# Optimization experiments

Measured on AMD Instinct MI355X. Metric: run time of the kernel, lower is better.

## Reference

```python
import jax, jax.numpy as jnp
import numpy as np

B, NQ, NKV, D = 2, 2048, 2048, 1024
N_HEADS = 16
D_H = D // N_HEADS


def setup_inputs() -> dict:
    key = jax.random.key(0)
    ks = jax.random.split(key, 10)
    s = 0.02  # weight init scale
    return {
        "q": jax.random.normal(ks[0], (B, NQ, D), jnp.float32),
        "kv": jax.random.normal(ks[1], (B, NKV, D), jnp.float32),
        "Wq": jax.random.normal(ks[2], (D, D), jnp.float32) * s,
        "bq": jnp.zeros((D,), jnp.float32),
        "Wk": jax.random.normal(ks[3], (D, D), jnp.float32) * s,
        "bk": jnp.zeros((D,), jnp.float32),
        "Wv": jax.random.normal(ks[4], (D, D), jnp.float32) * s,
        "bv": jnp.zeros((D,), jnp.float32),
        "Wo": jax.random.normal(ks[5], (D, D), jnp.float32) * s,
        "bo": jnp.zeros((D,), jnp.float32),
    }


def reference(q, kv, Wq, bq, Wk, bk, Wv, bv, Wo, bo):
    # Linear projections (torch Linear: x @ W.T + b)
    qh = q @ Wq.T + bq   # [B, NQ, D]
    kh = kv @ Wk.T + bk  # [B, NKV, D]
    vh = kv @ Wv.T + bv  # [B, NKV, D]
    # Split heads: [B, N, H, d_h]
    qh = qh.reshape(B, NQ, N_HEADS, D_H)
    kh = kh.reshape(B, NKV, N_HEADS, D_H)
    vh = vh.reshape(B, NKV, N_HEADS, D_H)
    scale = 1.0 / jnp.sqrt(jnp.asarray(D_H, qh.dtype))
    # QK^T per head: [B, H, NQ, NKV]
    scores = jnp.einsum("bqhd,bkhd->bhqk", qh, kh) * scale
    att = jax.nn.softmax(scores, axis=-1)
    # dropout p=0.0 -> identity
    out = jnp.einsum("bhqk,bkhd->bqhd", att, vh)  # [B, NQ, H, d_h]
    out = out.reshape(B, NQ, D)
    return out @ Wo.T + bo
```

## Files before the change

### kernel.cpp

```cpp
#include <hip/hip_runtime.h>
#include <cstddef>
#include <cstdint>

using half4v  = __attribute__((ext_vector_type(4))) _Float16;
using half8   = __attribute__((ext_vector_type(8))) _Float16;
using floatx4 = __attribute__((ext_vector_type(4))) float;

#define B_   2
#define NQ_  2048
#define DM   1024
#define NH_  16
#define DH_  64
#define NTILES 32

__device__ __forceinline__ void async16(const _Float16* g, _Float16* l) {
    __builtin_amdgcn_global_load_lds(
        (const __attribute__((address_space(1))) unsigned int*)g,
        (__attribute__((address_space(3))) unsigned int*)l, 16, 0, 0);
}

__global__ __launch_bounds__(256) void cvt_all(
        const float* __restrict__ q,  const float* __restrict__ kv,
        const float* __restrict__ wq, const float* __restrict__ wk,
        const float* __restrict__ wv, const float* __restrict__ wo,
        _Float16* __restrict__ dq,  _Float16* __restrict__ dkv,
        _Float16* __restrict__ dwq, _Float16* __restrict__ dwk,
        _Float16* __restrict__ dwv, _Float16* __restrict__ dwo) {
    int blk = blockIdx.x;
    const float* s;
    _Float16* d;
    int base;
    if (blk < 2048)      { s = q;  d = dq;  base = blk; }
    else if (blk < 4096) { s = kv; d = dkv; base = blk - 2048; }
    else if (blk < 4608) { s = wq; d = dwq; base = blk - 4096; }
    else if (blk < 5120) { s = wk; d = dwk; base = blk - 4608; }
    else if (blk < 5632) { s = wv; d = dwv; base = blk - 5120; }
    else                 { s = wo; d = dwo; base = blk - 5632; }
    int i = base * 256 + threadIdx.x;
    const float4* s4 = (const float4*)s;
    float4 a = s4[2 * i], b = s4[2 * i + 1];
    half8 h;
    h[0] = (_Float16)a.x; h[1] = (_Float16)a.y; h[2] = (_Float16)a.z; h[3] = (_Float16)a.w;
    h[4] = (_Float16)b.x; h[5] = (_Float16)b.y; h[6] = (_Float16)b.z; h[7] = (_Float16)b.w;
    ((half8*)d)[i] = h;
}

__global__ __launch_bounds__(256, 3) void proj_qkv(
        const _Float16* __restrict__ q16, const _Float16* __restrict__ kv16,
        const _Float16* __restrict__ wqp, const _Float16* __restrict__ wkp,
        const _Float16* __restrict__ wvp,
        const float* __restrict__ bqp, const float* __restrict__ bkp,
        const float* __restrict__ bvp,
        _Float16* __restrict__ qh, _Float16* __restrict__ kh,
        _Float16* __restrict__ vt) {
    __shared__ _Float16 As[128 * 64];
    __shared__ _Float16 Bs[128 * 64];

    const int which = blockIdx.x >> 8;
    const int sub = blockIdx.x & 255;
    const _Float16* A = (which == 0) ? q16 : kv16;
    const _Float16* W = (which == 0) ? wqp : (which == 1) ? wkp : wvp;
    const float* bias = (which == 0) ? bqp : (which == 1) ? bkp : bvp;

    const int t = threadIdx.x;
    const int w = t >> 6, lane = t & 63;
    const int r16 = lane & 15, quad = lane >> 4;
    const int bn = sub & 7, bm = sub >> 3;
    const int m0 = bm * 128, n0 = bn * 128;
    const int wm = w >> 1, wn = w & 1;

    floatx4 acc[4][4];
#pragma unroll
    for (int i = 0; i < 4; i++)
#pragma unroll
        for (int j = 0; j < 4; j++)
#pragma unroll
            for (int r = 0; r < 4; r++) acc[i][j][r] = 0.f;

    const int ph0 = quad ^ (r16 & 7), ph1 = ph0 ^ 4;

    for (int k0 = 0; k0 < DM; k0 += 64) {
        __syncthreads();
#pragma unroll
        for (int i = 0; i < 4; i++) {
            int P = i * 256 + t;
            int m = P >> 3, c = (P & 7) ^ (m & 7);
            async16(A + (size_t)(m0 + m) * DM + k0 + c * 8, &As[P * 8]);
            async16(W + (size_t)(n0 + m) * DM + k0 + c * 8, &Bs[P * 8]);
        }
        asm volatile("s_waitcnt vmcnt(0)" ::: "memory");
        __syncthreads();

        half8 af[4][2], bf[4][2];
#pragma unroll
        for (int mi = 0; mi < 4; mi++) {
            int m = wm * 64 + mi * 16 + r16;
            af[mi][0] = ((const half8*)As)[m * 8 + ph0];
            af[mi][1] = ((const half8*)As)[m * 8 + ph1];
        }
#pragma unroll
        for (int ni = 0; ni < 4; ni++) {
            int n = wn * 64 + ni * 16 + r16;
            bf[ni][0] = ((const half8*)Bs)[n * 8 + ph0];
            bf[ni][1] = ((const half8*)Bs)[n * 8 + ph1];
        }
#pragma unroll
        for (int kd = 0; kd < 2; kd++)
#pragma unroll
            for (int mi = 0; mi < 4; mi++)
#pragma unroll
                for (int ni = 0; ni < 4; ni++)
                    acc[mi][ni] = __builtin_amdgcn_mfma_f32_16x16x32_f16(
                        af[mi][kd], bf[ni][kd], acc[mi][ni], 0, 0, 0);
    }

    if (which < 2) {
        _Float16* C = (which == 0) ? qh : kh;
        const float esc = (which == 0) ? 0.125f : 1.0f;
#pragma unroll
        for (int mi = 0; mi < 4; mi++)
#pragma unroll
            for (int r = 0; r < 4; r++) {
                int row = m0 + wm * 64 + mi * 16 + quad * 4 + r;
#pragma unroll
                for (int ni = 0; ni < 4; ni++) {
                    int col = n0 + wn * 64 + ni * 16 + r16;
                    C[(size_t)row * DM + col] = (_Float16)((acc[mi][ni][r] + bias[col]) * esc);
                }
            }
    } else {
#pragma unroll
        for (int mi = 0; mi < 4; mi++) {
            int krow = m0 + wm * 64 + mi * 16 + quad * 4;
            int bb = krow >> 11, kk = krow & 2047;
#pragma unroll
            for (int ni = 0; ni < 4; ni++) {
                int col = n0 + wn * 64 + ni * 16 + r16;
                int hh = col >> 6, dd = col & 63;
                float bv = bias[col];
                half4v pk;
#pragma unroll
                for (int r = 0; r < 4; r++) pk[r] = (_Float16)(acc[mi][ni][r] + bv);
                *(half4v*)&vt[((size_t)((bb * NH_ + hh) * DH_ + dd)) * NQ_ + kk] = pk;
            }
        }
    }
}

__global__ __launch_bounds__(256, 2) void attn_mfma(const _Float16* __restrict__ Qg,
                                                    const _Float16* __restrict__ Kg,
                                                    const _Float16* __restrict__ Vt,
                                                    _Float16* __restrict__ Og) {
    __shared__ _Float16 Ps[128 * 64];
    __shared__ _Float16 Ks[2][64 * 64];
    __shared__ _Float16 Vs[2][64 * 64];

    const int t = threadIdx.x, w = t >> 6, lane = t & 63;
    const int r16 = lane & 15, quad = lane >> 4;
    const int qt = blockIdx.x & 15;
    const int bh = blockIdx.x >> 4;
    const int b = bh >> 4, h = bh & 15;

    const _Float16* qbase = Qg + (size_t)(b * NQ_ + qt * 128) * DM + h * DH_;
    const _Float16* kbase = Kg + (size_t)(b * NQ_) * DM + h * DH_;
    const _Float16* vbase = Vt + (size_t)bh * DH_ * NQ_;

#pragma unroll
    for (int i = 0; i < 4; i++) {
        int P = i * 256 + t;
        int m = P >> 3, c = (P & 7) ^ (m & 7);
        async16(qbase + (size_t)m * DM + c * 8, &Ps[P * 8]);
    }
#pragma unroll
    for (int i = 0; i < 2; i++) {
        int P = i * 256 + t;
        int m = P >> 3, c = (P & 7) ^ (m & 7);
        async16(kbase + (size_t)m * DM + c * 8, &Ks[0][P * 8]);
        async16(vbase + (size_t)m * NQ_ + c * 8, &Vs[0][P * 8]);
    }
    asm volatile("s_waitcnt vmcnt(0)" ::: "memory");
    __syncthreads();

    const int ph0 = quad ^ (r16 & 7), ph1 = ph0 ^ 4;
    half8 Qf[2][2];
#pragma unroll
    for (int mi = 0; mi < 2; mi++) {
        int m = w * 32 + mi * 16 + r16;
        Qf[mi][0] = ((const half8*)Ps)[m * 8 + ph0];
        Qf[mi][1] = ((const half8*)Ps)[m * 8 + ph1];
    }

    floatx4 oaccT[2][4];
    float lacc[2] = {0.f, 0.f};
#pragma unroll
    for (int mi = 0; mi < 2; mi++)
#pragma unroll
        for (int nd = 0; nd < 4; nd++)
#pragma unroll
            for (int r = 0; r < 4; r++) oaccT[mi][nd][r] = 0.f;

    for (int kt = 0; kt < NTILES; kt++) {
        const int cur = kt & 1;
        asm volatile("s_waitcnt vmcnt(0)" ::: "memory");
        __syncthreads();

        if (kt + 1 < NTILES) {
            const int nxt = cur ^ 1;
#pragma unroll
            for (int i = 0; i < 2; i++) {
                int P = i * 256 + t;
                int m = P >> 3, c = (P & 7) ^ (m & 7);
                async16(kbase + (size_t)((kt + 1) * 64 + m) * DM + c * 8, &Ks[nxt][P * 8]);
                async16(vbase + (size_t)m * NQ_ + (kt + 1) * 64 + c * 8, &Vs[nxt][P * 8]);
            }
        }

        floatx4 sacc[2][4];
#pragma unroll
        for (int mi = 0; mi < 2; mi++)
#pragma unroll
            for (int nk = 0; nk < 4; nk++)
#pragma unroll
                for (int r = 0; r < 4; r++) sacc[mi][nk][r] = 0.f;
#pragma unroll
        for (int kd = 0; kd < 2; kd++)
#pragma unroll
            for (int nk = 0; nk < 4; nk++) {
                half8 kf = ((const half8*)Ks[cur])[(nk * 16 + r16) * 8 + (kd ? ph1 : ph0)];
                sacc[0][nk] = __builtin_amdgcn_mfma_f32_16x16x32_f16(kf, Qf[0][kd], sacc[0][nk], 0, 0, 0);
                sacc[1][nk] = __builtin_amdgcn_mfma_f32_16x16x32_f16(kf, Qf[1][kd], sacc[1][nk], 0, 0, 0);
            }

#pragma unroll
        for (int mi = 0; mi < 2; mi++) {
            int q = w * 32 + mi * 16 + r16;
#pragma unroll
            for (int nk = 0; nk < 4; nk++) {
                float p0 = __expf(sacc[mi][nk][0]);
                float p1 = __expf(sacc[mi][nk][1]);
                float p2 = __expf(sacc[mi][nk][2]);
                float p3 = __expf(sacc[mi][nk][3]);
                lacc[mi] += (p0 + p1) + (p2 + p3);
                half4v pk;
                pk[0] = (_Float16)p0; pk[1] = (_Float16)p1;
                pk[2] = (_Float16)p2; pk[3] = (_Float16)p3;
                int phys = (nk * 2 + (quad >> 1)) ^ (r16 & 7);
                *(half4v*)&Ps[q * 64 + phys * 8 + (quad & 1) * 4] = pk;
            }
        }

#pragma unroll
        for (int ks = 0; ks < 2; ks++) {
            half8 pf[2];
#pragma unroll
            for (int mi = 0; mi < 2; mi++) {
                int q = w * 32 + mi * 16 + r16;
                pf[mi] = ((const half8*)Ps)[q * 8 + ((ks * 4 + quad) ^ (r16 & 7))];
            }
#pragma unroll
            for (int nd = 0; nd < 4; nd++) {
                half8 vf = ((const half8*)Vs[cur])[(nd * 16 + r16) * 8 + ((ks * 4 + quad) ^ (r16 & 7))];
                oaccT[0][nd] = __builtin_amdgcn_mfma_f32_16x16x32_f16(vf, pf[0], oaccT[0][nd], 0, 0, 0);
                oaccT[1][nd] = __builtin_amdgcn_mfma_f32_16x16x32_f16(vf, pf[1], oaccT[1][nd], 0, 0, 0);
            }
        }
    }

#pragma unroll
    for (int mi = 0; mi < 2; mi++) {
        float l = lacc[mi];
        l += __shfl_xor(l, 16);
        l += __shfl_xor(l, 32);
        float inv = 1.f / l;
        int qrow = b * NQ_ + qt * 128 + w * 32 + mi * 16 + r16;
#pragma unroll
        for (int nd = 0; nd < 4; nd++) {
            half4v o;
#pragma unroll
            for (int r = 0; r < 4; r++) o[r] = (_Float16)(oaccT[mi][nd][r] * inv);
            *(half4v*)&Og[(size_t)qrow * DM + h * DH_ + nd * 16 + quad * 4] = o;
        }
    }
}

__global__ __launch_bounds__(256, 2) void gemm_o(const _Float16* __restrict__ A,
                                                 const _Float16* __restrict__ W,
                                                 const float* __restrict__ bias,
                                                 float* __restrict__ C) {
    __shared__ _Float16 As[128 * 64];
    __shared__ _Float16 Bs[64 * 64];

    const int t = threadIdx.x;
    const int w = t >> 6, lane = t & 63;
    const int r16 = lane & 15, quad = lane >> 4;
    const int bn = blockIdx.x & 15, bm = blockIdx.x >> 4;
    const int m0 = bm * 128, n0 = bn * 64;
    const int wm = w >> 1, wn = w & 1;

    floatx4 acc[4][2];
#pragma unroll
    for (int i = 0; i < 4; i++)
#pragma unroll
        for (int j = 0; j < 2; j++)
#pragma unroll
            for (int r = 0; r < 4; r++) acc[i][j][r] = 0.f;

    const int ph0 = quad ^ (r16 & 7), ph1 = ph0 ^ 4;

    for (int k0 = 0; k0 < DM; k0 += 64) {
        __syncthreads();
#pragma unroll
        for (int i = 0; i < 4; i++) {
            int P = i * 256 + t;
            int m = P >> 3, c = (P & 7) ^ (m & 7);
            async16(A + (size_t)(m0 + m) * DM + k0 + c * 8, &As[P * 8]);
        }
#pragma unroll
        for (int i = 0; i < 2; i++) {
            int P = i * 256 + t;
            int m = P >> 3, c = (P & 7) ^ (m & 7);
            async16(W + (size_t)(n0 + m) * DM + k0 + c * 8, &Bs[P * 8]);
        }
        asm volatile("s_waitcnt vmcnt(0)" ::: "memory");
        __syncthreads();

        half8 af[4][2], bf[2][2];
#pragma unroll
        for (int mi = 0; mi < 4; mi++) {
            int m = wm * 64 + mi * 16 + r16;
            af[mi][0] = ((const half8*)As)[m * 8 + ph0];
            af[mi][1] = ((const half8*)As)[m * 8 + ph1];
        }
#pragma unroll
        for (int ni = 0; ni < 2; ni++) {
            int n = wn * 32 + ni * 16 + r16;
            bf[ni][0] = ((const half8*)Bs)[n * 8 + ph0];
            bf[ni][1] = ((const half8*)Bs)[n * 8 + ph1];
        }
#pragma unroll
        for (int kd = 0; kd < 2; kd++)
#pragma unroll
            for (int mi = 0; mi < 4; mi++)
#pragma unroll
                for (int ni = 0; ni < 2; ni++)
                    acc[mi][ni] = __builtin_amdgcn_mfma_f32_16x16x32_f16(
                        af[mi][kd], bf[ni][kd], acc[mi][ni], 0, 0, 0);
    }

#pragma unroll
    for (int mi = 0; mi < 4; mi++)
#pragma unroll
        for (int r = 0; r < 4; r++) {
            int row = m0 + wm * 64 + mi * 16 + quad * 4 + r;
#pragma unroll
            for (int ni = 0; ni < 2; ni++) {
                int col = n0 + wn * 32 + ni * 16 + r16;
                C[(size_t)row * DM + col] = acc[mi][ni][r] + bias[col];
            }
        }
}

extern "C" void kernel_launch(void* const* d_in, const int* in_sizes, int n_in,
                              void* d_out, int out_size, void* d_ws, size_t ws_size,
                              hipStream_t stream) {
    const float* q  = (const float*)d_in[0];
    const float* kv = (const float*)d_in[1];
    const float* Wq = (const float*)d_in[2];
    const float* bq = (const float*)d_in[3];
    const float* Wk = (const float*)d_in[4];
    const float* bk = (const float*)d_in[5];
    const float* Wv = (const float*)d_in[6];
    const float* bv = (const float*)d_in[7];
    const float* Wo = (const float*)d_in[8];
    const float* bo = (const float*)d_in[9];

    char* ws = (char*)d_ws;
    _Float16* q16  = (_Float16*)(ws);
    _Float16* kv16 = (_Float16*)(ws + (size_t)(8  << 20));
    _Float16* w16q = (_Float16*)(ws + (size_t)(16 << 20));
    _Float16* w16k = (_Float16*)(ws + (size_t)(18 << 20));
    _Float16* w16v = (_Float16*)(ws + (size_t)(20 << 20));
    _Float16* w16o = (_Float16*)(ws + (size_t)(22 << 20));
    _Float16* qh16 = (_Float16*)(ws + (size_t)(24 << 20));
    _Float16* kh16 = (_Float16*)(ws + (size_t)(32 << 20));
    _Float16* vt16 = (_Float16*)(ws + (size_t)(40 << 20));
    _Float16* ao16 = (_Float16*)(ws + (size_t)(48 << 20));

    cvt_all<<<6144, 256, 0, stream>>>(q, kv, Wq, Wk, Wv, Wo,
                                      q16, kv16, w16q, w16k, w16v, w16o);

    proj_qkv<<<768, 256, 0, stream>>>(q16, kv16, w16q, w16k, w16v,
                                      bq, bk, bv, qh16, kh16, vt16);

    attn_mfma<<<512, 256, 0, stream>>>(qh16, kh16, vt16, ao16);

    gemm_o<<<512, 256, 0, stream>>>(ao16, w16o, bo, (float*)d_out);
}
```

Measured before the change: 215.2 us.

## Halve attention and output GEMM tiles, double grids, remap block order

The attention kernel now handles 64 query rows per block instead of 128, and the output-projection GEMM uses 64x64 tiles instead of 128x64. Both grids double to 1024 blocks and launch bounds rise to 4 blocks per CU. Block indices are remapped in attention, gemm_o and proj_qkv so that neighbouring blocks spread across heads or row tiles, which should improve spreading across the XCDs and cache locality. The aim is more parallelism and occupancy on the many CUs. In exchange each K/V tile is reused by fewer query rows, so global/L2 traffic per FLOP rises and the MFMA-to-LDS-load ratio drops.

```diff
diff --git a/kernel.cpp b/kernel.cpp
--- a/kernel.cpp
+++ b/kernel.cpp
@@ -65,7 +65,8 @@
     const int t = threadIdx.x;
     const int w = t >> 6, lane = t & 63;
     const int r16 = lane & 15, quad = lane >> 4;
-    const int bn = sub & 7, bm = sub >> 3;
+    const int bm = (sub & 7) * 4 + ((sub >> 3) & 3);
+    const int bn = sub >> 5;
     const int m0 = bm * 128, n0 = bn * 128;
     const int wm = w >> 1, wn = w & 1;
 
@@ -147,34 +148,30 @@
     }
 }
 
-__global__ __launch_bounds__(256, 2) void attn_mfma(const _Float16* __restrict__ Qg,
+__global__ __launch_bounds__(256, 4) void attn_mfma(const _Float16* __restrict__ Qg,
                                                     const _Float16* __restrict__ Kg,
                                                     const _Float16* __restrict__ Vt,
                                                     _Float16* __restrict__ Og) {
-    __shared__ _Float16 Ps[128 * 64];
+    __shared__ _Float16 Ps[64 * 64];
     __shared__ _Float16 Ks[2][64 * 64];
     __shared__ _Float16 Vs[2][64 * 64];
 
     const int t = threadIdx.x, w = t >> 6, lane = t & 63;
     const int r16 = lane & 15, quad = lane >> 4;
-    const int qt = blockIdx.x & 15;
-    const int bh = blockIdx.x >> 4;
+    const int blk = blockIdx.x;
+    const int bh = (blk & 7) * 4 + ((blk >> 3) & 3);
+    const int qt = blk >> 5;
     const int b = bh >> 4, h = bh & 15;
 
-    const _Float16* qbase = Qg + (size_t)(b * NQ_ + qt * 128) * DM + h * DH_;
+    const _Float16* qbase = Qg + (size_t)(b * NQ_ + qt * 64) * DM + h * DH_;
     const _Float16* kbase = Kg + (size_t)(b * NQ_) * DM + h * DH_;
     const _Float16* vbase = Vt + (size_t)bh * DH_ * NQ_;
 
 #pragma unroll
-    for (int i = 0; i < 4; i++) {
+    for (int i = 0; i < 2; i++) {
         int P = i * 256 + t;
         int m = P >> 3, c = (P & 7) ^ (m & 7);
         async16(qbase + (size_t)m * DM + c * 8, &Ps[P * 8]);
-    }
-#pragma unroll
-    for (int i = 0; i < 2; i++) {
-        int P = i * 256 + t;
-        int m = P >> 3, c = (P & 7) ^ (m & 7);
         async16(kbase + (size_t)m * DM + c * 8, &Ks[0][P * 8]);
         async16(vbase + (size_t)m * NQ_ + c * 8, &Vs[0][P * 8]);
     }
@@ -182,22 +179,19 @@
     __syncthreads();
 
     const int ph0 = quad ^ (r16 & 7), ph1 = ph0 ^ 4;
-    half8 Qf[2][2];
-#pragma unroll
-    for (int mi = 0; mi < 2; mi++) {
-        int m = w * 32 + mi * 16 + r16;
-        Qf[mi][0] = ((const half8*)Ps)[m * 8 + ph0];
-        Qf[mi][1] = ((const half8*)Ps)[m * 8 + ph1];
-    }
-
-    floatx4 oaccT[2][4];
-    float lacc[2] = {0.f, 0.f};
-#pragma unroll
-    for (int mi = 0; mi < 2; mi++)
-#pragma unroll
-        for (int nd = 0; nd < 4; nd++)
-#pragma unroll
-            for (int r = 0; r < 4; r++) oaccT[mi][nd][r] = 0.f;
+    half8 Qf[2];
+    {
+        int m = w * 16 + r16;
+        Qf[0] = ((const half8*)Ps)[m * 8 + ph0];
+        Qf[1] = ((const half8*)Ps)[m * 8 + ph1];
+    }
+
+    floatx4 oaccT[4];
+    float lacc = 0.f;
+#pragma unroll
+    for (int nd = 0; nd < 4; nd++)
+#pragma unroll
+        for (int r = 0; r < 4; r++) oaccT[nd][r] = 0.f;
 
     for (int kt = 0; kt < NTILES; kt++) {
         const int cur = kt & 1;
@@ -215,91 +209,80 @@
             }
         }
 
-        floatx4 sacc[2][4];
-#pragma unroll
-        for (int mi = 0; mi < 2; mi++)
-#pragma unroll
-            for (int nk = 0; nk < 4; nk++)
-#pragma unroll
-                for (int r = 0; r < 4; r++) sacc[mi][nk][r] = 0.f;
+        floatx4 sacc[4];
+#pragma unroll
+        for (int nk = 0; nk < 4; nk++)
+#pragma unroll
+            for (int r = 0; r < 4; r++) sacc[nk][r] = 0.f;
 #pragma unroll
         for (int kd = 0; kd < 2; kd++)
 #pragma unroll
             for (int nk = 0; nk < 4; nk++) {
                 half8 kf = ((const half8*)Ks[cur])[(nk * 16 + r16) * 8 + (kd ? ph1 : ph0)];
-                sacc[0][nk] = __builtin_amdgcn_mfma_f32_16x16x32_f16(kf, Qf[0][kd], sacc[0][nk], 0, 0, 0);
-                sacc[1][nk] = __builtin_amdgcn_mfma_f32_16x16x32_f16(kf, Qf[1][kd], sacc[1][nk], 0, 0, 0);
-            }
-
-#pragma unroll
-        for (int mi = 0; mi < 2; mi++) {
-            int q = w * 32 + mi * 16 + r16;
-#pragma unroll
-            for (int nk = 0; nk < 4; nk++) {
-                float p0 = __expf(sacc[mi][nk][0]);
-                float p1 = __expf(sacc[mi][nk][1]);
-                float p2 = __expf(sacc[mi][nk][2]);
-                float p3 = __expf(sacc[mi][nk][3]);
-                lacc[mi] += (p0 + p1) + (p2 + p3);
-                half4v pk;
-                pk[0] = (_Float16)p0; pk[1] = (_Float16)p1;
-                pk[2] = (_Float16)p2; pk[3] = (_Float16)p3;
-                int phys = (nk * 2 + (quad >> 1)) ^ (r16 & 7);
-                *(half4v*)&Ps[q * 64 + phys * 8 + (quad & 1) * 4] = pk;
-            }
+                sacc[nk] = __builtin_amdgcn_mfma_f32_16x16x32_f16(kf, Qf[kd], sacc[nk], 0, 0, 0);
+            }
+
+        const int q = w * 16 + r16;
+#pragma unroll
+        for (int nk = 0; nk < 4; nk++) {
+            float p0 = __expf(sacc[nk][0]);
+            float p1 = __expf(sacc[nk][1]);
+            float p2 = __expf(sacc[nk][2]);
+            float p3 = __expf(sacc[nk][3]);
+            lacc += (p0 + p1) + (p2 + p3);
+            half4v pk;
+            pk[0] = (_Float16)p0; pk[1] = (_Float16)p1;
+            pk[2] = (_Float16)p2; pk[3] = (_Float16)p3;
+            int phys = (nk * 2 + (quad >> 1)) ^ (r16 & 7);
+            *(half4v*)&Ps[q * 64 + phys * 8 + (quad & 1) * 4] = pk;
         }
 
 #pragma unroll
         for (int ks = 0; ks < 2; ks++) {
-            half8 pf[2];
-#pragma unroll
-            for (int mi = 0; mi < 2; mi++) {
-                int q = w * 32 + mi * 16 + r16;
-                pf[mi] = ((const half8*)Ps)[q * 8 + ((ks * 4 + quad) ^ (r16 & 7))];
-            }
+            half8 pf = ((const half8*)Ps)[q * 8 + ((ks * 4 + quad) ^ (r16 & 7))];
 #pragma unroll
             for (int nd = 0; nd < 4; nd++) {
                 half8 vf = ((const half8*)Vs[cur])[(nd * 16 + r16) * 8 + ((ks * 4 + quad) ^ (r16 & 7))];
-                oaccT[0][nd] = __builtin_amdgcn_mfma_f32_16x16x32_f16(vf, pf[0], oaccT[0][nd], 0, 0, 0);
-                oaccT[1][nd] = __builtin_amdgcn_mfma_f32_16x16x32_f16(vf, pf[1], oaccT[1][nd], 0, 0, 0);
-            }
-        }
-    }
-
-#pragma unroll
-    for (int mi = 0; mi < 2; mi++) {
-        float l = lacc[mi];
+                oaccT[nd] = __builtin_amdgcn_mfma_f32_16x16x32_f16(vf, pf, oaccT[nd], 0, 0, 0);
+            }
+        }
+    }
+
+    {
+        float l = lacc;
         l += __shfl_xor(l, 16);
         l += __shfl_xor(l, 32);
         float inv = 1.f / l;
-        int qrow = b * NQ_ + qt * 128 + w * 32 + mi * 16 + r16;
+        int qrow = b * NQ_ + qt * 64 + w * 16 + r16;
 #pragma unroll
         for (int nd = 0; nd < 4; nd++) {
             half4v o;
 #pragma unroll
-            for (int r = 0; r < 4; r++) o[r] = (_Float16)(oaccT[mi][nd][r] * inv);
+            for (int r = 0; r < 4; r++) o[r] = (_Float16)(oaccT[nd][r] * inv);
             *(half4v*)&Og[(size_t)qrow * DM + h * DH_ + nd * 16 + quad * 4] = o;
         }
     }
 }
 
-__global__ __launch_bounds__(256, 2) void gemm_o(const _Float16* __restrict__ A,
+__global__ __launch_bounds__(256, 4) void gemm_o(const _Float16* __restrict__ A,
                                                  const _Float16* __restrict__ W,
                                                  const float* __restrict__ bias,
                                                  float* __restrict__ C) {
-    __shared__ _Float16 As[128 * 64];
+    __shared__ _Float16 As[64 * 64];
     __shared__ _Float16 Bs[64 * 64];
 
     const int t = threadIdx.x;
     const int w = t >> 6, lane = t & 63;
     const int r16 = lane & 15, quad = lane >> 4;
-    const int bn = blockIdx.x & 15, bm = blockIdx.x >> 4;
-    const int m0 = bm * 128, n0 = bn * 64;
+    const int blk = blockIdx.x;
+    const int bm = (blk & 7) * 8 + ((blk >> 3) & 7);
+    const int bn = blk >> 6;
+    const int m0 = bm * 64, n0 = bn * 64;
     const int wm = w >> 1, wn = w & 1;
 
-    floatx4 acc[4][2];
-#pragma unroll
-    for (int i = 0; i < 4; i++)
+    floatx4 acc[2][2];
+#pragma unroll
+    for (int i = 0; i < 2; i++)
 #pragma unroll
         for (int j = 0; j < 2; j++)
 #pragma unroll
@@ -310,24 +293,19 @@
     for (int k0 = 0; k0 < DM; k0 += 64) {
         __syncthreads();
 #pragma unroll
-        for (int i = 0; i < 4; i++) {
+        for (int i = 0; i < 2; i++) {
             int P = i * 256 + t;
             int m = P >> 3, c = (P & 7) ^ (m & 7);
             async16(A + (size_t)(m0 + m) * DM + k0 + c * 8, &As[P * 8]);
-        }
-#pragma unroll
-        for (int i = 0; i < 2; i++) {
-            int P = i * 256 + t;
-            int m = P >> 3, c = (P & 7) ^ (m & 7);
             async16(W + (size_t)(n0 + m) * DM + k0 + c * 8, &Bs[P * 8]);
         }
         asm volatile("s_waitcnt vmcnt(0)" ::: "memory");
         __syncthreads();
 
-        half8 af[4][2], bf[2][2];
-#pragma unroll
-        for (int mi = 0; mi < 4; mi++) {
-            int m = wm * 64 + mi * 16 + r16;
+        half8 af[2][2], bf[2][2];
+#pragma unroll
+        for (int mi = 0; mi < 2; mi++) {
+            int m = wm * 32 + mi * 16 + r16;
             af[mi][0] = ((const half8*)As)[m * 8 + ph0];
             af[mi][1] = ((const half8*)As)[m * 8 + ph1];
         }
@@ -340,7 +318,7 @@
 #pragma unroll
         for (int kd = 0; kd < 2; kd++)
 #pragma unroll
-            for (int mi = 0; mi < 4; mi++)
+            for (int mi = 0; mi < 2; mi++)
 #pragma unroll
                 for (int ni = 0; ni < 2; ni++)
                     acc[mi][ni] = __builtin_amdgcn_mfma_f32_16x16x32_f16(
@@ -348,10 +326,10 @@
     }
 
 #pragma unroll
-    for (int mi = 0; mi < 4; mi++)
+    for (int mi = 0; mi < 2; mi++)
 #pragma unroll
         for (int r = 0; r < 4; r++) {
-            int row = m0 + wm * 64 + mi * 16 + quad * 4 + r;
+            int row = m0 + wm * 32 + mi * 16 + quad * 4 + r;
 #pragma unroll
             for (int ni = 0; ni < 2; ni++) {
                 int col = n0 + wn * 32 + ni * 16 + r16;
@@ -392,7 +370,7 @@
     proj_qkv<<<768, 256, 0, stream>>>(q16, kv16, w16q, w16k, w16v,
                                       bq, bk, bv, qh16, kh16, vt16);
 
-    attn_mfma<<<512, 256, 0, stream>>>(qh16, kh16, vt16, ao16);
-
-    gemm_o<<<512, 256, 0, stream>>>(ao16, w16o, bo, (float*)d_out);
-}
+    attn_mfma<<<1024, 256, 0, stream>>>(qh16, kh16, vt16, ao16);
+
+    gemm_o<<<1024, 256, 0, stream>>>(ao16, w16o, bo, (float*)d_out);
+}
```

After: 198.6 us. 7.7% less time.
